# Kernel optimization log

Hardware: AMD Instinct MI355X
Metric: run time of the kernel (lower is better)

## Reference

```python
import jax, jax.numpy as jnp
import numpy as np

N_NODES = 100000
N_EDGES = 1600000
N_GRAPHS = 512
NODE_DIM = 64   # len(node_indices)
GRAPH_DIM = 16  # len(graph_indices) == graph_channels
HIDDEN = 128
OUT = 8


def setup_inputs() -> dict:
    key = jax.random.key(0)
    ks = jax.random.split(key, 12)
    x = jax.random.normal(ks[0], (N_NODES, NODE_DIM + GRAPH_DIM), dtype=jnp.float32)
    edge_index = jax.random.randint(ks[1], (2, N_EDGES), 0, N_NODES, dtype=jnp.int64)
    batch = jnp.sort(jax.random.randint(ks[2], (N_NODES,), 0, N_GRAPHS, dtype=jnp.int64))
    def lin(k, fan_in, fan_out):
        lim = 1.0 / np.sqrt(fan_in)
        return jax.random.uniform(k, (fan_in, fan_out), jnp.float32, -lim, lim)
    return {
        "x": x, "edge_index": edge_index, "batch": batch,
        "W1": lin(ks[3], NODE_DIM, HIDDEN), "b1": jnp.zeros((HIDDEN,), jnp.float32),
        "W2": lin(ks[4], HIDDEN, HIDDEN),   "b2": jnp.zeros((HIDDEN,), jnp.float32),
        "Wm1": lin(ks[5], HIDDEN + GRAPH_DIM, HIDDEN), "bm1": jnp.zeros((HIDDEN,), jnp.float32),
        "Wm2": lin(ks[6], HIDDEN, OUT), "bm2": jnp.zeros((OUT,), jnp.float32),
    }


def _gcn_conv(h_in, src, dst, W, b):
    # PyG GCNConv: h = X W; out = D^{-1/2}(A+I)D^{-1/2} h + b, deg over A+I.
    h = h_in @ W                                        # [N, H]
    deg = jnp.zeros((N_NODES,), h.dtype).at[dst].add(1.0) + 1.0  # +1 self loop
    dinv = jax.lax.rsqrt(deg)                           # [N]
    norm = dinv[src] * dinv[dst]                        # [E]
    out = jnp.zeros_like(h).at[dst].add(norm[:, None] * h[src])
    out = out + (dinv * dinv)[:, None] * h              # self-loop term
    return out + b


def _mean_pool(v, batch):
    cnt = jax.ops.segment_sum(jnp.ones((v.shape[0],), v.dtype), batch, num_segments=N_GRAPHS)
    s = jax.ops.segment_sum(v, batch, num_segments=N_GRAPHS)
    return s / jnp.maximum(cnt, 1.0)[:, None]


def reference(x, edge_index, batch, W1, b1, W2, b2, Wm1, bm1, Wm2, bm2):
    src, dst = edge_index[0], edge_index[1]
    node_t = x[:, :NODE_DIM]                 # node_indices slice
    graph_t = _mean_pool(x[:, NODE_DIM:], batch)  # graph_indices slice, pooled [G, 16]
    h = _gcn_conv(node_t, src, dst, W1, b1)
    h = jax.nn.relu(h)                       # dropout is identity in eval mode
    h = _gcn_conv(h, src, dst, W2, b2)
    g = _mean_pool(h, batch)                 # [G, H]
    g = jnp.concatenate([g, graph_t], axis=1)
    g = jax.nn.relu(g @ Wm1 + bm1)
    return g @ Wm2 + bm2                     # [G, OUT]
```

## Files before the change

### kernel.cpp

```cpp
#include <hip/hip_runtime.h>
#include <hip/hip_bf16.h>

#define N_NODES 100000
#define N_EDGES 1600000
#define N_GRAPHS 512
#define NODE_DIM 64
#define GRAPH_DIM 16
#define HIDDEN 128
#define OUT_DIM 8

#define NBUCKETS 391
#define BIN_CAP 8192
#define EPB 4096

__device__ __forceinline__ float bflo(unsigned u) { return __uint_as_float(u << 16); }
__device__ __forceinline__ float bfhi(unsigned u) { return __uint_as_float(u & 0xffff0000u); }


__global__ __launch_bounds__(256) void k_binplace(const int* __restrict__ src,
                                                  const int* __restrict__ dst,
                                                  int* __restrict__ gcur,
                                                  unsigned* __restrict__ bin) {
    __shared__ int cnt[NBUCKETS];
    __shared__ int base[NBUCKETS];
    int t = threadIdx.x;
    for (int i = t; i < NBUCKETS; i += 256) cnt[i] = 0;
    __syncthreads();
    int e0 = blockIdx.x * EPB;
#pragma unroll
    for (int k = 0; k < EPB / 256; k++) {
        int e = e0 + k * 256 + t;
        if (e < N_EDGES) atomicAdd(&cnt[dst[e] >> 8], 1);
    }
    __syncthreads();
    for (int i = t; i < NBUCKETS; i += 256) {
        int c = cnt[i];
        base[i] = (c > 0) ? atomicAdd(&gcur[i], c) : 0;
        cnt[i] = 0;
    }
    __syncthreads();
#pragma unroll
    for (int k = 0; k < EPB / 256; k++) {
        int e = e0 + k * 256 + t;
        if (e < N_EDGES) {
            int d = dst[e];
            int b = d >> 8;
            int p = atomicAdd(&cnt[b], 1);
            bin[(size_t)b * BIN_CAP + base[b] + p] = ((unsigned)src[e] << 8) | (unsigned)(d & 255);
        }
    }
}


__global__ __launch_bounds__(256) void k_degBf(const int* __restrict__ gcur,
                                               const unsigned* __restrict__ bin,
                                               int* __restrict__ degcnt,
                                               float* __restrict__ dinv,
                                               int* __restrict__ bsum) {
    __shared__ int cnt[256];
    int b = blockIdx.x, t = threadIdx.x;
    cnt[t] = 0;
    __syncthreads();
    int n = gcur[b];
    const unsigned* seg = bin + (size_t)b * BIN_CAP;
    for (int i = t; i < n; i += 256) atomicAdd(&cnt[seg[i] & 255u], 1);
    __syncthreads();
    int c = cnt[t];
    int node = b * 256 + t;
    if (node < N_NODES) {
        degcnt[node] = c;
        dinv[node] = rsqrtf((float)c + 1.0f);
    }
    __syncthreads();
    for (int o = 128; o > 0; o >>= 1) {
        if (t < o) cnt[t] += cnt[t + o];
        __syncthreads();
    }
    if (t == 0) bsum[b] = cnt[0];
}


__global__ __launch_bounds__(512) void k_scanb(const int* __restrict__ bsum,
                                               int* __restrict__ bofs) {
    __shared__ int s[512];
    int t = threadIdx.x;
    int v = (t < NBUCKETS) ? bsum[t] : 0;
    s[t] = v;
    __syncthreads();
    for (int o = 1; o < 512; o <<= 1) {
        int u = (t >= o) ? s[t - o] : 0;
        __syncthreads();
        s[t] += u;
        __syncthreads();
    }
    if (t < NBUCKETS) bofs[t] = s[t] - v;
}


__global__ __launch_bounds__(256) void k_rowfill(const int* __restrict__ degcnt,
                                                 const int* __restrict__ bofs,
                                                 const int* __restrict__ gcur,
                                                 const unsigned* __restrict__ bin,
                                                 const float* __restrict__ dinv,
                                                 int* __restrict__ row_start,
                                                 int2* __restrict__ csre,
                                                 float* __restrict__ gt_sum) {
    __shared__ int sc[256];
    __shared__ int rsl[256];
    __shared__ int cnt[256];
    __shared__ float dl[256];
    int b = blockIdx.x, t = threadIdx.x;
    if (b < 32) gt_sum[b * 256 + t] = 0.0f;
    int node = b * 256 + t;
    int v = (node < N_NODES) ? degcnt[node] : 0;
    sc[t] = v;
    __syncthreads();
    for (int o = 1; o < 256; o <<= 1) {
        int u = (t >= o) ? sc[t - o] : 0;
        __syncthreads();
        sc[t] += u;
        __syncthreads();
    }
    int rs = bofs[b] + sc[t] - v;
    if (node < N_NODES) row_start[node] = rs;
    rsl[t] = rs;
    cnt[t] = 0;
    dl[t] = rsqrtf((float)v + 1.0f);
    __syncthreads();
    int n = gcur[b];
    const unsigned* seg = bin + (size_t)b * BIN_CAP;
    for (int i = t; i < n; i += 256) {
        unsigned e = seg[i];
        int dlidx = (int)(e & 255u);
        int s = (int)(e >> 8);
        int pos = rsl[dlidx] + atomicAdd(&cnt[dlidx], 1);
        csre[pos] = make_int2(s, __float_as_int(dinv[s] * dl[dlidx]));
    }
}


__global__ __launch_bounds__(256) void k_packstat(const float* __restrict__ x,
                                                  const int* __restrict__ batch,
                                                  ushort* __restrict__ xb,
                                                  float* __restrict__ gt_sum) {
    int t = threadIdx.x;
    int i0 = blockIdx.x * 64;
    for (int idx = t; idx < 64 * 32; idx += 256) {
        int node = i0 + (idx >> 5);
        if (node < N_NODES) {
            int c2 = idx & 31;
            float2 v = *(const float2*)&x[(size_t)node * 80 + c2 * 2];
            __hip_bfloat16 lo = __float2bfloat16(v.x);
            __hip_bfloat16 hi = __float2bfloat16(v.y);
            ushort2 pv = make_ushort2(*(ushort*)&lo, *(ushort*)&hi);
            ((ushort2*)xb)[(size_t)node * 32 + c2] = pv;
        }
    }
    int c = t & 15, sub = t >> 4;
    int iend = min(i0 + 64, N_NODES);
    float acc = 0.0f;
    int g = -1;
    for (int i = i0 + sub; i < iend; i += 16) {
        int bi = batch[i];
        if (bi != g) {
            if (g >= 0) atomicAdd(&gt_sum[g * GRAPH_DIM + c], acc);
            acc = 0.0f; g = bi;
        }
        acc += x[(size_t)i * 80 + NODE_DIM + c];
    }
    if (g >= 0) atomicAdd(&gt_sum[g * GRAPH_DIM + c], acc);
}


#define LDX(s_) __uint_as_float((unsigned)xb[(size_t)(s_)*64 + lane] << 16)

__global__ __launch_bounds__(256) void k_conv1(const int2* __restrict__ csre,
                                               const int* __restrict__ row_start,
                                               const float* __restrict__ dinv,
                                               const ushort* __restrict__ xb,
                                               const float* __restrict__ W,
                                               const float* __restrict__ bias,
                                               ushort* __restrict__ C,
                                               float* __restrict__ gsum2) {
    __shared__ float zs[8][64];
    int t = threadIdx.x;
    if (blockIdx.x < 256) gsum2[blockIdx.x * 256 + t] = 0.0f;
    int w = t >> 6, lane = t & 63;
    int nA = blockIdx.x * 8 + w * 2;
    int nB = nA + 1;
    int rsA = row_start[nA], reA = (nA == N_NODES - 1) ? N_EDGES : row_start[nA + 1];
    int rsB = row_start[nB], reB = (nB == N_NODES - 1) ? N_EDGES : row_start[nB + 1];
    float aA0 = 0.f, aA1 = 0.f, aA2 = 0.f, aA3 = 0.f;
    float aB0 = 0.f, aB1 = 0.f, aB2 = 0.f, aB3 = 0.f;
    int kA = rsA, kB = rsB;
    while (kA + 4 <= reA && kB + 4 <= reB) {
        int2 eA0 = csre[kA], eA1 = csre[kA + 1], eA2 = csre[kA + 2], eA3 = csre[kA + 3];
        int2 eB0 = csre[kB], eB1 = csre[kB + 1], eB2 = csre[kB + 2], eB3 = csre[kB + 3];
        float vA0 = LDX(eA0.x), vA1 = LDX(eA1.x), vA2 = LDX(eA2.x), vA3 = LDX(eA3.x);
        float vB0 = LDX(eB0.x), vB1 = LDX(eB1.x), vB2 = LDX(eB2.x), vB3 = LDX(eB3.x);
        aA0 += __int_as_float(eA0.y) * vA0; aA1 += __int_as_float(eA1.y) * vA1;
        aA2 += __int_as_float(eA2.y) * vA2; aA3 += __int_as_float(eA3.y) * vA3;
        aB0 += __int_as_float(eB0.y) * vB0; aB1 += __int_as_float(eB1.y) * vB1;
        aB2 += __int_as_float(eB2.y) * vB2; aB3 += __int_as_float(eB3.y) * vB3;
        kA += 4; kB += 4;
    }
    while (kA + 4 <= reA) {
        int2 e0 = csre[kA], e1 = csre[kA + 1], e2 = csre[kA + 2], e3 = csre[kA + 3];
        float v0 = LDX(e0.x), v1 = LDX(e1.x), v2 = LDX(e2.x), v3 = LDX(e3.x);
        aA0 += __int_as_float(e0.y) * v0; aA1 += __int_as_float(e1.y) * v1;
        aA2 += __int_as_float(e2.y) * v2; aA3 += __int_as_float(e3.y) * v3;
        kA += 4;
    }
    while (kB + 4 <= reB) {
        int2 e0 = csre[kB], e1 = csre[kB + 1], e2 = csre[kB + 2], e3 = csre[kB + 3];
        float v0 = LDX(e0.x), v1 = LDX(e1.x), v2 = LDX(e2.x), v3 = LDX(e3.x);
        aB0 += __int_as_float(e0.y) * v0; aB1 += __int_as_float(e1.y) * v1;
        aB2 += __int_as_float(e2.y) * v2; aB3 += __int_as_float(e3.y) * v3;
        kB += 4;
    }
    while (kA < reA && kB < reB) {
        int2 eA = csre[kA]; int2 eB = csre[kB];
        aA0 += __int_as_float(eA.y) * LDX(eA.x);
        aB0 += __int_as_float(eB.y) * LDX(eB.x);
        kA++; kB++;
    }
    while (kA < reA) { int2 e = csre[kA]; aA0 += __int_as_float(e.y) * LDX(e.x); kA++; }
    while (kB < reB) { int2 e = csre[kB]; aB0 += __int_as_float(e.y) * LDX(e.x); kB++; }
    float dA = dinv[nA], dB = dinv[nB];
    zs[w * 2][lane]     = aA0 + aA1 + aA2 + aA3 + dA * dA * LDX(nA);
    zs[w * 2 + 1][lane] = aB0 + aB1 + aB2 + aB3 + dB * dB * LDX(nB);
    __syncthreads();
    if (t < 128) {
        int j = t;
        float acc[8];
#pragma unroll
        for (int m = 0; m < 8; m++) acc[m] = 0.0f;
        for (int k = 0; k < 64; k++) {
            float wv = W[k * 128 + j];
#pragma unroll
            for (int m = 0; m < 8; m++) acc[m] += zs[m][k] * wv;
        }
        float b = bias[j];
        size_t row0 = (size_t)blockIdx.x * 8;
#pragma unroll
        for (int m = 0; m < 8; m++) {
            float v = fmaxf(acc[m] + b, 0.0f);
            __hip_bfloat16 hv = __float2bfloat16(v);
            C[(row0 + m) * 128 + j] = *(ushort*)&hv;
        }
    }
}


__global__ __launch_bounds__(256) void k_gather2(const int2* __restrict__ csre,
                                                 const int* __restrict__ row_start,
                                                 const float* __restrict__ dinv,
                                                 const unsigned* __restrict__ h,
                                                 const int* __restrict__ batch,
                                                 float* __restrict__ gsum2) {
    __shared__ float2 red[8][64];
    int w = threadIdx.x >> 6, lane = threadIdx.x & 63;
    int nA = blockIdx.x * 8 + w * 2;
    int nB = nA + 1;
    int rsA = row_start[nA], reA = (nA == N_NODES - 1) ? N_EDGES : row_start[nA + 1];
    int rsB = row_start[nB], reB = (nB == N_NODES - 1) ? N_EDGES : row_start[nB + 1];
    float2 aA0 = {0.f,0.f}, aA1 = {0.f,0.f}, aA2 = {0.f,0.f}, aA3 = {0.f,0.f};
    float2 aB0 = {0.f,0.f}, aB1 = {0.f,0.f}, aB2 = {0.f,0.f}, aB3 = {0.f,0.f};
    int kA = rsA, kB = rsB;
#define FMA2(acc_, wbits_, u_) { float w_ = __int_as_float(wbits_); \
                             acc_.x += w_ * bflo(u_); acc_.y += w_ * bfhi(u_); }
    while (kA + 4 <= reA && kB + 4 <= reB) {
        int2 eA0 = csre[kA], eA1 = csre[kA + 1], eA2 = csre[kA + 2], eA3 = csre[kA + 3];
        int2 eB0 = csre[kB], eB1 = csre[kB + 1], eB2 = csre[kB + 2], eB3 = csre[kB + 3];
        unsigned uA0 = h[(size_t)eA0.x * 64 + lane], uA1 = h[(size_t)eA1.x * 64 + lane];
        unsigned uA2 = h[(size_t)eA2.x * 64 + lane], uA3 = h[(size_t)eA3.x * 64 + lane];
        unsigned uB0 = h[(size_t)eB0.x * 64 + lane], uB1 = h[(size_t)eB1.x * 64 + lane];
        unsigned uB2 = h[(size_t)eB2.x * 64 + lane], uB3 = h[(size_t)eB3.x * 64 + lane];
        FMA2(aA0, eA0.y, uA0); FMA2(aA1, eA1.y, uA1); FMA2(aA2, eA2.y, uA2); FMA2(aA3, eA3.y, uA3);
        FMA2(aB0, eB0.y, uB0); FMA2(aB1, eB1.y, uB1); FMA2(aB2, eB2.y, uB2); FMA2(aB3, eB3.y, uB3);
        kA += 4; kB += 4;
    }
    while (kA + 4 <= reA) {
        int2 e0 = csre[kA], e1 = csre[kA + 1], e2 = csre[kA + 2], e3 = csre[kA + 3];
        unsigned u0 = h[(size_t)e0.x * 64 + lane], u1 = h[(size_t)e1.x * 64 + lane];
        unsigned u2 = h[(size_t)e2.x * 64 + lane], u3 = h[(size_t)e3.x * 64 + lane];
        FMA2(aA0, e0.y, u0); FMA2(aA1, e1.y, u1); FMA2(aA2, e2.y, u2); FMA2(aA3, e3.y, u3);
        kA += 4;
    }
    while (kB + 4 <= reB) {
        int2 e0 = csre[kB], e1 = csre[kB + 1], e2 = csre[kB + 2], e3 = csre[kB + 3];
        unsigned u0 = h[(size_t)e0.x * 64 + lane], u1 = h[(size_t)e1.x * 64 + lane];
        unsigned u2 = h[(size_t)e2.x * 64 + lane], u3 = h[(size_t)e3.x * 64 + lane];
        FMA2(aB0, e0.y, u0); FMA2(aB1, e1.y, u1); FMA2(aB2, e2.y, u2); FMA2(aB3, e3.y, u3);
        kB += 4;
    }
    while (kA < reA && kB < reB) {
        int2 eA = csre[kA]; int2 eB = csre[kB];
        unsigned uA = h[(size_t)eA.x * 64 + lane], uB = h[(size_t)eB.x * 64 + lane];
        FMA2(aA0, eA.y, uA); FMA2(aB0, eB.y, uB);
        kA++; kB++;
    }
    while (kA < reA) {
        int2 e = csre[kA]; unsigned u = h[(size_t)e.x * 64 + lane];
        FMA2(aA0, e.y, u); kA++;
    }
    while (kB < reB) {
        int2 e = csre[kB]; unsigned u = h[(size_t)e.x * 64 + lane];
        FMA2(aB0, e.y, u); kB++;
    }
#undef FMA2
    float dA = dinv[nA], dB = dinv[nB];
    unsigned usA = h[(size_t)nA * 64 + lane];
    unsigned usB = h[(size_t)nB * 64 + lane];
    float2 rA, rB;
    rA.x = aA0.x + aA1.x + aA2.x + aA3.x + dA * dA * bflo(usA);
    rA.y = aA0.y + aA1.y + aA2.y + aA3.y + dA * dA * bfhi(usA);
    rB.x = aB0.x + aB1.x + aB2.x + aB3.x + dB * dB * bflo(usB);
    rB.y = aB0.y + aB1.y + aB2.y + aB3.y + dB * dB * bfhi(usB);
    red[w * 2][lane] = rA;
    red[w * 2 + 1][lane] = rB;
    __syncthreads();
    int g0 = batch[blockIdx.x * 8];
    int g7 = batch[blockIdx.x * 8 + 7];
    if (g0 == g7) {
        if (w == 0) {
            float sx = 0.f, sy = 0.f;
#pragma unroll
            for (int q = 0; q < 8; q++) { sx += red[q][lane].x; sy += red[q][lane].y; }
            atomicAdd(&gsum2[g0 * 128 + 2 * lane], sx);
            atomicAdd(&gsum2[g0 * 128 + 2 * lane + 1], sy);
        }
    } else {
        int gA = batch[nA], gB = batch[nB];
        atomicAdd(&gsum2[gA * 128 + 2 * lane], rA.x);
        atomicAdd(&gsum2[gA * 128 + 2 * lane + 1], rA.y);
        atomicAdd(&gsum2[gB * 128 + 2 * lane], rB.x);
        atomicAdd(&gsum2[gB * 128 + 2 * lane + 1], rB.y);
    }
}


__global__ __launch_bounds__(128) void k_mlp(const float* __restrict__ gsum2,
                                             const float* __restrict__ gt_sum,
                                             const int* __restrict__ batch,
                                             const float* __restrict__ W2,
                                             const float* __restrict__ b2,
                                             const float* __restrict__ Wm1,
                                             const float* __restrict__ bm1,
                                             const float* __restrict__ Wm2,
                                             const float* __restrict__ bm2,
                                             float* __restrict__ out) {
    __shared__ float srow[HIDDEN];
    __shared__ float g144[HIDDEN + GRAPH_DIM];
    __shared__ float sm[HIDDEN];
    __shared__ int cnt_sh;
    int b = blockIdx.x;
    int j = threadIdx.x;
    float raw = gsum2[b * 128 + j];
    float gtraw = (j < GRAPH_DIM) ? gt_sum[b * GRAPH_DIM + j] : 0.0f;
    if (j == 0) {
        int lo = 0, hi = N_NODES;
        while (lo < hi) { int m = (lo + hi) >> 1; if (batch[m] < b) lo = m + 1; else hi = m; }
        int a = lo;
        lo = 0; hi = N_NODES;
        while (lo < hi) { int m = (lo + hi) >> 1; if (batch[m] < b + 1) lo = m + 1; else hi = m; }
        cnt_sh = lo - a;
    }
    __syncthreads();
    float inv = 1.0f / fmaxf((float)cnt_sh, 1.0f);
    srow[j] = raw * inv;
    if (j < GRAPH_DIM) g144[128 + j] = gtraw * inv;
    __syncthreads();
    float z = b2[j];
    for (int k = 0; k < 128; k++) z += srow[k] * W2[k * 128 + j];
    g144[j] = z;
    __syncthreads();
    float acc = bm1[j];
    for (int k = 0; k < HIDDEN + GRAPH_DIM; k++) acc += g144[k] * Wm1[k * 128 + j];
    sm[j] = fmaxf(acc, 0.0f);
    __syncthreads();
    if (j < OUT_DIM) {
        float o = bm2[j];
        for (int k = 0; k < 128; k++) o += sm[k] * Wm2[k * OUT_DIM + j];
        out[b * OUT_DIM + j] = o;
    }
}

extern "C" void kernel_launch(void* const* d_in, const int* in_sizes, int n_in,
                              void* d_out, int out_size, void* d_ws, size_t ws_size,
                              hipStream_t stream) {
    const float* x    = (const float*)d_in[0];
    const int*   edge = (const int*)d_in[1];
    const int*   src  = edge;
    const int*   dst  = edge + N_EDGES;
    const int*   batch= (const int*)d_in[2];
    const float* W1   = (const float*)d_in[3];
    const float* b1   = (const float*)d_in[4];
    const float* W2   = (const float*)d_in[5];
    const float* b2   = (const float*)d_in[6];
    const float* Wm1  = (const float*)d_in[7];
    const float* bm1  = (const float*)d_in[8];
    const float* Wm2  = (const float*)d_in[9];
    const float* bm2  = (const float*)d_in[10];
    float* out = (float*)d_out;

    char* ws = (char*)d_ws;
    char* p = ws;
    unsigned* bin   = (unsigned*)p;  p += (size_t)NBUCKETS * BIN_CAP * 4;
    int2*  csre     = (int2*)p;      p += (size_t)N_EDGES * 8;
    ushort* h1b     = (ushort*)p;    p += (size_t)N_NODES * 128 * 2;
    ushort* xb      = (ushort*)p;    p += (size_t)N_NODES * 64 * 2;
    int*   degcnt   = (int*)p;       p += (size_t)NBUCKETS * 256 * 4;
    int*   row_start= (int*)p;       p += (size_t)N_NODES * 4;
    float* dinv     = (float*)p;     p += (size_t)N_NODES * 4;
    int*   gcur     = (int*)p;       p += (size_t)NBUCKETS * 4;
    int*   bsum     = (int*)p;       p += 512 * 4;
    int*   bofs     = (int*)p;       p += 512 * 4;
    float* gt_sum   = (float*)p;     p += (size_t)N_GRAPHS * GRAPH_DIM * 4;
    float* gsum2    = (float*)p;     p += (size_t)N_GRAPHS * 128 * 4;

    hipMemsetAsync(gcur, 0, (size_t)NBUCKETS * 4, stream);

    k_binplace<<<(N_EDGES + EPB - 1) / EPB, 256, 0, stream>>>(src, dst, gcur, bin);
    k_degBf<<<NBUCKETS, 256, 0, stream>>>(gcur, bin, degcnt, dinv, bsum);
    k_scanb<<<1, 512, 0, stream>>>(bsum, bofs);
    k_rowfill<<<NBUCKETS, 256, 0, stream>>>(degcnt, bofs, gcur, bin, dinv, row_start, csre, gt_sum);

    k_packstat<<<(N_NODES + 63) / 64, 256, 0, stream>>>(x, batch, xb, gt_sum);

    k_conv1<<<N_NODES / 8, 256, 0, stream>>>(csre, row_start, dinv, xb, W1, b1, h1b, gsum2);

    k_gather2<<<N_NODES / 8, 256, 0, stream>>>(csre, row_start, dinv,
                                               (const unsigned*)h1b, batch, gsum2);

    k_mlp<<<N_GRAPHS, 128, 0, stream>>>(gsum2, gt_sum, batch, W2, b2, Wm1, bm1, Wm2, bm2, out);
}
```

Before: 248.2 us.

## Fuse CSR build into one kernel with padded bucket rows and on-the-fly norms

Merges the degree count, block scan and row fill kernels into a single per-bucket build kernel. Rows now start at a fixed bucket offset (b*BIN_CAP) and are stored as start/end pairs, so no global scan is needed. The CSR stores only source indices, and the edge weight is recomputed in the gather kernels from dinv, which halves index traffic at the cost of an extra random dinv load per edge. The conv1 dense transform is also split across all 256 threads instead of 128.

Result: faster. 237.7 us (-4.2%).

```diff
diff --git a/kernel.cpp b/kernel.cpp
--- a/kernel.cpp
+++ b/kernel.cpp
@@ -52,68 +52,25 @@
 }
 
 
-__global__ __launch_bounds__(256) void k_degBf(const int* __restrict__ gcur,
+__global__ __launch_bounds__(256) void k_build(const int* __restrict__ gcur,
                                                const unsigned* __restrict__ bin,
-                                               int* __restrict__ degcnt,
                                                float* __restrict__ dinv,
-                                               int* __restrict__ bsum) {
+                                               int2* __restrict__ rowse,
+                                               int* __restrict__ csr,
+                                               float* __restrict__ gt_sum) {
     __shared__ int cnt[256];
+    __shared__ int sc[256];
+    __shared__ int rsl[256];
     int b = blockIdx.x, t = threadIdx.x;
+    if (b < 32) gt_sum[b * 256 + t] = 0.0f;
     cnt[t] = 0;
     __syncthreads();
     int n = gcur[b];
     const unsigned* seg = bin + (size_t)b * BIN_CAP;
     for (int i = t; i < n; i += 256) atomicAdd(&cnt[seg[i] & 255u], 1);
     __syncthreads();
-    int c = cnt[t];
-    int node = b * 256 + t;
-    if (node < N_NODES) {
-        degcnt[node] = c;
-        dinv[node] = rsqrtf((float)c + 1.0f);
-    }
-    __syncthreads();
-    for (int o = 128; o > 0; o >>= 1) {
-        if (t < o) cnt[t] += cnt[t + o];
-        __syncthreads();
-    }
-    if (t == 0) bsum[b] = cnt[0];
-}
-
-
-__global__ __launch_bounds__(512) void k_scanb(const int* __restrict__ bsum,
-                                               int* __restrict__ bofs) {
-    __shared__ int s[512];
-    int t = threadIdx.x;
-    int v = (t < NBUCKETS) ? bsum[t] : 0;
-    s[t] = v;
-    __syncthreads();
-    for (int o = 1; o < 512; o <<= 1) {
-        int u = (t >= o) ? s[t - o] : 0;
-        __syncthreads();
-        s[t] += u;
-        __syncthreads();
-    }
-    if (t < NBUCKETS) bofs[t] = s[t] - v;
-}
-
-
-__global__ __launch_bounds__(256) void k_rowfill(const int* __restrict__ degcnt,
-                                                 const int* __restrict__ bofs,
-                                                 const int* __restrict__ gcur,
-                                                 const unsigned* __restrict__ bin,
-                                                 const float* __restrict__ dinv,
-                                                 int* __restrict__ row_start,
-                                                 int2* __restrict__ csre,
-                                                 float* __restrict__ gt_sum) {
-    __shared__ int sc[256];
-    __shared__ int rsl[256];
-    __shared__ int cnt[256];
-    __shared__ float dl[256];
-    int b = blockIdx.x, t = threadIdx.x;
-    if (b < 32) gt_sum[b * 256 + t] = 0.0f;
-    int node = b * 256 + t;
-    int v = (node < N_NODES) ? degcnt[node] : 0;
-    sc[t] = v;
+    int deg = cnt[t];
+    sc[t] = deg;
     __syncthreads();
     for (int o = 1; o < 256; o <<= 1) {
         int u = (t >= o) ? sc[t - o] : 0;
@@ -121,20 +78,19 @@
         sc[t] += u;
         __syncthreads();
     }
-    int rs = bofs[b] + sc[t] - v;
-    if (node < N_NODES) row_start[node] = rs;
+    int rs = b * BIN_CAP + sc[t] - deg;
+    int node = b * 256 + t;
+    if (node < N_NODES) {
+        dinv[node] = rsqrtf((float)deg + 1.0f);
+        rowse[node] = make_int2(rs, rs + deg);
+    }
     rsl[t] = rs;
     cnt[t] = 0;
-    dl[t] = rsqrtf((float)v + 1.0f);
-    __syncthreads();
-    int n = gcur[b];
-    const unsigned* seg = bin + (size_t)b * BIN_CAP;
+    __syncthreads();
     for (int i = t; i < n; i += 256) {
         unsigned e = seg[i];
         int dlidx = (int)(e & 255u);
-        int s = (int)(e >> 8);
-        int pos = rsl[dlidx] + atomicAdd(&cnt[dlidx], 1);
-        csre[pos] = make_int2(s, __float_as_int(dinv[s] * dl[dlidx]));
+        csr[rsl[dlidx] + atomicAdd(&cnt[dlidx], 1)] = (int)(e >> 8);
     }
 }
 
@@ -174,8 +130,8 @@
 
 #define LDX(s_) __uint_as_float((unsigned)xb[(size_t)(s_)*64 + lane] << 16)
 
-__global__ __launch_bounds__(256) void k_conv1(const int2* __restrict__ csre,
-                                               const int* __restrict__ row_start,
+__global__ __launch_bounds__(256) void k_conv1(const int* __restrict__ csr,
+                                               const int2* __restrict__ rowse,
                                                const float* __restrict__ dinv,
                                                const ushort* __restrict__ xb,
                                                const float* __restrict__ W,
@@ -188,62 +144,64 @@
     int w = t >> 6, lane = t & 63;
     int nA = blockIdx.x * 8 + w * 2;
     int nB = nA + 1;
-    int rsA = row_start[nA], reA = (nA == N_NODES - 1) ? N_EDGES : row_start[nA + 1];
-    int rsB = row_start[nB], reB = (nB == N_NODES - 1) ? N_EDGES : row_start[nB + 1];
+    int2 seA = rowse[nA];
+    int2 seB = rowse[nB];
+    int kA = seA.x, reA = seA.y;
+    int kB = seB.x, reB = seB.y;
+    float dA = dinv[nA], dB = dinv[nB];
     float aA0 = 0.f, aA1 = 0.f, aA2 = 0.f, aA3 = 0.f;
     float aB0 = 0.f, aB1 = 0.f, aB2 = 0.f, aB3 = 0.f;
-    int kA = rsA, kB = rsB;
     while (kA + 4 <= reA && kB + 4 <= reB) {
-        int2 eA0 = csre[kA], eA1 = csre[kA + 1], eA2 = csre[kA + 2], eA3 = csre[kA + 3];
-        int2 eB0 = csre[kB], eB1 = csre[kB + 1], eB2 = csre[kB + 2], eB3 = csre[kB + 3];
-        float vA0 = LDX(eA0.x), vA1 = LDX(eA1.x), vA2 = LDX(eA2.x), vA3 = LDX(eA3.x);
-        float vB0 = LDX(eB0.x), vB1 = LDX(eB1.x), vB2 = LDX(eB2.x), vB3 = LDX(eB3.x);
-        aA0 += __int_as_float(eA0.y) * vA0; aA1 += __int_as_float(eA1.y) * vA1;
-        aA2 += __int_as_float(eA2.y) * vA2; aA3 += __int_as_float(eA3.y) * vA3;
-        aB0 += __int_as_float(eB0.y) * vB0; aB1 += __int_as_float(eB1.y) * vB1;
-        aB2 += __int_as_float(eB2.y) * vB2; aB3 += __int_as_float(eB3.y) * vB3;
+        int a0 = csr[kA], a1 = csr[kA + 1], a2 = csr[kA + 2], a3 = csr[kA + 3];
+        int b0 = csr[kB], b1 = csr[kB + 1], b2 = csr[kB + 2], b3 = csr[kB + 3];
+        float wa0 = dinv[a0] * dA, wa1 = dinv[a1] * dA, wa2 = dinv[a2] * dA, wa3 = dinv[a3] * dA;
+        float wb0 = dinv[b0] * dB, wb1 = dinv[b1] * dB, wb2 = dinv[b2] * dB, wb3 = dinv[b3] * dB;
+        float vA0 = LDX(a0), vA1 = LDX(a1), vA2 = LDX(a2), vA3 = LDX(a3);
+        float vB0 = LDX(b0), vB1 = LDX(b1), vB2 = LDX(b2), vB3 = LDX(b3);
+        aA0 += wa0 * vA0; aA1 += wa1 * vA1; aA2 += wa2 * vA2; aA3 += wa3 * vA3;
+        aB0 += wb0 * vB0; aB1 += wb1 * vB1; aB2 += wb2 * vB2; aB3 += wb3 * vB3;
         kA += 4; kB += 4;
     }
     while (kA + 4 <= reA) {
-        int2 e0 = csre[kA], e1 = csre[kA + 1], e2 = csre[kA + 2], e3 = csre[kA + 3];
-        float v0 = LDX(e0.x), v1 = LDX(e1.x), v2 = LDX(e2.x), v3 = LDX(e3.x);
-        aA0 += __int_as_float(e0.y) * v0; aA1 += __int_as_float(e1.y) * v1;
-        aA2 += __int_as_float(e2.y) * v2; aA3 += __int_as_float(e3.y) * v3;
+        int a0 = csr[kA], a1 = csr[kA + 1], a2 = csr[kA + 2], a3 = csr[kA + 3];
+        float wa0 = dinv[a0] * dA, wa1 = dinv[a1] * dA, wa2 = dinv[a2] * dA, wa3 = dinv[a3] * dA;
+        float v0 = LDX(a0), v1 = LDX(a1), v2 = LDX(a2), v3 = LDX(a3);
+        aA0 += wa0 * v0; aA1 += wa1 * v1; aA2 += wa2 * v2; aA3 += wa3 * v3;
         kA += 4;
     }
     while (kB + 4 <= reB) {
-        int2 e0 = csre[kB], e1 = csre[kB + 1], e2 = csre[kB + 2], e3 = csre[kB + 3];
-        float v0 = LDX(e0.x), v1 = LDX(e1.x), v2 = LDX(e2.x), v3 = LDX(e3.x);
-        aB0 += __int_as_float(e0.y) * v0; aB1 += __int_as_float(e1.y) * v1;
-        aB2 += __int_as_float(e2.y) * v2; aB3 += __int_as_float(e3.y) * v3;
+        int b0 = csr[kB], b1 = csr[kB + 1], b2 = csr[kB + 2], b3 = csr[kB + 3];
+        float wb0 = dinv[b0] * dB, wb1 = dinv[b1] * dB, wb2 = dinv[b2] * dB, wb3 = dinv[b3] * dB;
+        float v0 = LDX(b0), v1 = LDX(b1), v2 = LDX(b2), v3 = LDX(b3);
+        aB0 += wb0 * v0; aB1 += wb1 * v1; aB2 += wb2 * v2; aB3 += wb3 * v3;
         kB += 4;
     }
     while (kA < reA && kB < reB) {
-        int2 eA = csre[kA]; int2 eB = csre[kB];
-        aA0 += __int_as_float(eA.y) * LDX(eA.x);
-        aB0 += __int_as_float(eB.y) * LDX(eB.x);
+        int a0 = csr[kA]; int b0 = csr[kB];
+        aA0 += dinv[a0] * dA * LDX(a0);
+        aB0 += dinv[b0] * dB * LDX(b0);
         kA++; kB++;
     }
-    while (kA < reA) { int2 e = csre[kA]; aA0 += __int_as_float(e.y) * LDX(e.x); kA++; }
-    while (kB < reB) { int2 e = csre[kB]; aB0 += __int_as_float(e.y) * LDX(e.x); kB++; }
-    float dA = dinv[nA], dB = dinv[nB];
+    while (kA < reA) { int a0 = csr[kA]; aA0 += dinv[a0] * dA * LDX(a0); kA++; }
+    while (kB < reB) { int b0 = csr[kB]; aB0 += dinv[b0] * dB * LDX(b0); kB++; }
     zs[w * 2][lane]     = aA0 + aA1 + aA2 + aA3 + dA * dA * LDX(nA);
     zs[w * 2 + 1][lane] = aB0 + aB1 + aB2 + aB3 + dB * dB * LDX(nB);
     __syncthreads();
-    if (t < 128) {
-        int j = t;
-        float acc[8];
-#pragma unroll
-        for (int m = 0; m < 8; m++) acc[m] = 0.0f;
+    {
+        int j = t & 127;
+        int hf = t >> 7;
+        float acc[4];
+#pragma unroll
+        for (int m = 0; m < 4; m++) acc[m] = 0.0f;
         for (int k = 0; k < 64; k++) {
-            float wv = W[k * 128 + j];
-#pragma unroll
-            for (int m = 0; m < 8; m++) acc[m] += zs[m][k] * wv;
+            float wk = W[k * 128 + j];
+#pragma unroll
+            for (int m = 0; m < 4; m++) acc[m] += zs[hf * 4 + m][k] * wk;
         }
         float b = bias[j];
-        size_t row0 = (size_t)blockIdx.x * 8;
-#pragma unroll
-        for (int m = 0; m < 8; m++) {
+        size_t row0 = (size_t)blockIdx.x * 8 + hf * 4;
+#pragma unroll
+        for (int m = 0; m < 4; m++) {
             float v = fmaxf(acc[m] + b, 0.0f);
             __hip_bfloat16 hv = __float2bfloat16(v);
             C[(row0 + m) * 128 + j] = *(ushort*)&hv;
@@ -252,8 +210,8 @@
 }
 
 
-__global__ __launch_bounds__(256) void k_gather2(const int2* __restrict__ csre,
-                                                 const int* __restrict__ row_start,
+__global__ __launch_bounds__(256) void k_gather2(const int* __restrict__ csr,
+                                                 const int2* __restrict__ rowse,
                                                  const float* __restrict__ dinv,
                                                  const unsigned* __restrict__ h,
                                                  const int* __restrict__ batch,
@@ -262,54 +220,61 @@
     int w = threadIdx.x >> 6, lane = threadIdx.x & 63;
     int nA = blockIdx.x * 8 + w * 2;
     int nB = nA + 1;
-    int rsA = row_start[nA], reA = (nA == N_NODES - 1) ? N_EDGES : row_start[nA + 1];
-    int rsB = row_start[nB], reB = (nB == N_NODES - 1) ? N_EDGES : row_start[nB + 1];
+    int2 seA = rowse[nA];
+    int2 seB = rowse[nB];
+    int kA = seA.x, reA = seA.y;
+    int kB = seB.x, reB = seB.y;
+    float dA = dinv[nA], dB = dinv[nB];
     float2 aA0 = {0.f,0.f}, aA1 = {0.f,0.f}, aA2 = {0.f,0.f}, aA3 = {0.f,0.f};
     float2 aB0 = {0.f,0.f}, aB1 = {0.f,0.f}, aB2 = {0.f,0.f}, aB3 = {0.f,0.f};
-    int kA = rsA, kB = rsB;
-#define FMA2(acc_, wbits_, u_) { float w_ = __int_as_float(wbits_); \
-                             acc_.x += w_ * bflo(u_); acc_.y += w_ * bfhi(u_); }
+#define FMA2(acc_, w_, u_) { acc_.x += (w_) * bflo(u_); acc_.y += (w_) * bfhi(u_); }
     while (kA + 4 <= reA && kB + 4 <= reB) {
-        int2 eA0 = csre[kA], eA1 = csre[kA + 1], eA2 = csre[kA + 2], eA3 = csre[kA + 3];
-        int2 eB0 = csre[kB], eB1 = csre[kB + 1], eB2 = csre[kB + 2], eB3 = csre[kB + 3];
-        unsigned uA0 = h[(size_t)eA0.x * 64 + lane], uA1 = h[(size_t)eA1.x * 64 + lane];
-        unsigned uA2 = h[(size_t)eA2.x * 64 + lane], uA3 = h[(size_t)eA3.x * 64 + lane];
-        unsigned uB0 = h[(size_t)eB0.x * 64 + lane], uB1 = h[(size_t)eB1.x * 64 + lane];
-        unsigned uB2 = h[(size_t)eB2.x * 64 + lane], uB3 = h[(size_t)eB3.x * 64 + lane];
-        FMA2(aA0, eA0.y, uA0); FMA2(aA1, eA1.y, uA1); FMA2(aA2, eA2.y, uA2); FMA2(aA3, eA3.y, uA3);
-        FMA2(aB0, eB0.y, uB0); FMA2(aB1, eB1.y, uB1); FMA2(aB2, eB2.y, uB2); FMA2(aB3, eB3.y, uB3);
+        int a0 = csr[kA], a1 = csr[kA + 1], a2 = csr[kA + 2], a3 = csr[kA + 3];
+        int b0 = csr[kB], b1 = csr[kB + 1], b2 = csr[kB + 2], b3 = csr[kB + 3];
+        float wa0 = dinv[a0] * dA, wa1 = dinv[a1] * dA, wa2 = dinv[a2] * dA, wa3 = dinv[a3] * dA;
+        float wb0 = dinv[b0] * dB, wb1 = dinv[b1] * dB, wb2 = dinv[b2] * dB, wb3 = dinv[b3] * dB;
+        unsigned uA0 = h[(size_t)a0 * 64 + lane], uA1 = h[(size_t)a1 * 64 + lane];
+        unsigned uA2 = h[(size_t)a2 * 64 + lane], uA3 = h[(size_t)a3 * 64 + lane];
+        unsigned uB0 = h[(size_t)b0 * 64 + lane], uB1 = h[(size_t)b1 * 64 + lane];
+        unsigned uB2 = h[(size_t)b2 * 64 + lane], uB3 = h[(size_t)b3 * 64 + lane];
+        FMA2(aA0, wa0, uA0); FMA2(aA1, wa1, uA1); FMA2(aA2, wa2, uA2); FMA2(aA3, wa3, uA3);
+        FMA2(aB0, wb0, uB0); FMA2(aB1, wb1, uB1); FMA2(aB2, wb2, uB2); FMA2(aB3, wb3, uB3);
         kA += 4; kB += 4;
     }
     while (kA + 4 <= reA) {
-        int2 e0 = csre[kA], e1 = csre[kA + 1], e2 = csre[kA + 2], e3 = csre[kA + 3];
-        unsigned u0 = h[(size_t)e0.x * 64 + lane], u1 = h[(size_t)e1.x * 64 + lane];
-        unsigned u2 = h[(size_t)e2.x * 64 + lane], u3 = h[(size_t)e3.x * 64 + lane];
-        FMA2(aA0, e0.y, u0); FMA2(aA1, e1.y, u1); FMA2(aA2, e2.y, u2); FMA2(aA3, e3.y, u3);
+        int a0 = csr[kA], a1 = csr[kA + 1], a2 = csr[kA + 2], a3 = csr[kA + 3];
+        float wa0 = dinv[a0] * dA, wa1 = dinv[a1] * dA, wa2 = dinv[a2] * dA, wa3 = dinv[a3] * dA;
+        unsigned u0 = h[(size_t)a0 * 64 + lane], u1 = h[(size_t)a1 * 64 + lane];
+        unsigned u2 = h[(size_t)a2 * 64 + lane], u3 = h[(size_t)a3 * 64 + lane];
+        FMA2(aA0, wa0, u0); FMA2(aA1, wa1, u1); FMA2(aA2, wa2, u2); FMA2(aA3, wa3, u3);
         kA += 4;
     }
     while (kB + 4 <= reB) {
-        int2 e0 = csre[kB], e1 = csre[kB + 1], e2 = csre[kB + 2], e3 = csre[kB + 3];
-        unsigned u0 = h[(size_t)e0.x * 64 + lane], u1 = h[(size_t)e1.x * 64 + lane];
-        unsigned u2 = h[(size_t)e2.x * 64 + lane], u3 = h[(size_t)e3.x * 64 + lane];
-        FMA2(aB0, e0.y, u0); FMA2(aB1, e1.y, u1); FMA2(aB2, e2.y, u2); FMA2(aB3, e3.y, u3);
+        int b0 = csr[kB], b1 = csr[kB + 1], b2 = csr[kB + 2], b3 = csr[kB + 3];
+        float wb0 = dinv[b0] * dB, wb1 = dinv[b1] * dB, wb2 = dinv[b2] * dB, wb3 = dinv[b3] * dB;
+        unsigned u0 = h[(size_t)b0 * 64 + lane], u1 = h[(size_t)b1 * 64 + lane];
+        unsigned u2 = h[(size_t)b2 * 64 + lane], u3 = h[(size_t)b3 * 64 + lane];
+        FMA2(aB0, wb0, u0); FMA2(aB1, wb1, u1); FMA2(aB2, wb2, u2); FMA2(aB3, wb3, u3);
         kB += 4;
     }
     while (kA < reA && kB < reB) {
-        int2 eA = csre[kA]; int2 eB = csre[kB];
-        unsigned uA = h[(size_t)eA.x * 64 + lane], uB = h[(size_t)eB.x * 64 + lane];
-        FMA2(aA0, eA.y, uA); FMA2(aB0, eB.y, uB);
+        int a0 = csr[kA]; int b0 = csr[kB];
+        float wa0 = dinv[a0] * dA, wb0 = dinv[b0] * dB;
+        unsigned uA = h[(size_t)a0 * 64 + lane], uB = h[(size_t)b0 * 64 + lane];
+        FMA2(aA0, wa0, uA); FMA2(aB0, wb0, uB);
         kA++; kB++;
     }
     while (kA < reA) {
-        int2 e = csre[kA]; unsigned u = h[(size_t)e.x * 64 + lane];
-        FMA2(aA0, e.y, u); kA++;
+        int a0 = csr[kA];
+        unsigned u = h[(size_t)a0 * 64 + lane];
+        FMA2(aA0, dinv[a0] * dA, u); kA++;
     }
     while (kB < reB) {
-        int2 e = csre[kB]; unsigned u = h[(size_t)e.x * 64 + lane];
-        FMA2(aB0, e.y, u); kB++;
+        int b0 = csr[kB];
+        unsigned u = h[(size_t)b0 * 64 + lane];
+        FMA2(aB0, dinv[b0] * dB, u); kB++;
     }
 #undef FMA2
-    float dA = dinv[nA], dB = dinv[nB];
     unsigned usA = h[(size_t)nA * 64 + lane];
     unsigned usB = h[(size_t)nB * 64 + lane];
     float2 rA, rB;
@@ -407,30 +372,25 @@
     char* ws = (char*)d_ws;
     char* p = ws;
     unsigned* bin   = (unsigned*)p;  p += (size_t)NBUCKETS * BIN_CAP * 4;
-    int2*  csre     = (int2*)p;      p += (size_t)N_EDGES * 8;
+    int*   csr      = (int*)p;       p += (size_t)NBUCKETS * BIN_CAP * 4;
     ushort* h1b     = (ushort*)p;    p += (size_t)N_NODES * 128 * 2;
     ushort* xb      = (ushort*)p;    p += (size_t)N_NODES * 64 * 2;
-    int*   degcnt   = (int*)p;       p += (size_t)NBUCKETS * 256 * 4;
-    int*   row_start= (int*)p;       p += (size_t)N_NODES * 4;
+    int2*  rowse    = (int2*)p;      p += (size_t)N_NODES * 8;
     float* dinv     = (float*)p;     p += (size_t)N_NODES * 4;
     int*   gcur     = (int*)p;       p += (size_t)NBUCKETS * 4;
-    int*   bsum     = (int*)p;       p += 512 * 4;
-    int*   bofs     = (int*)p;       p += 512 * 4;
     float* gt_sum   = (float*)p;     p += (size_t)N_GRAPHS * GRAPH_DIM * 4;
     float* gsum2    = (float*)p;     p += (size_t)N_GRAPHS * 128 * 4;
 
     hipMemsetAsync(gcur, 0, (size_t)NBUCKETS * 4, stream);
 
     k_binplace<<<(N_EDGES + EPB - 1) / EPB, 256, 0, stream>>>(src, dst, gcur, bin);
-    k_degBf<<<NBUCKETS, 256, 0, stream>>>(gcur, bin, degcnt, dinv, bsum);
-    k_scanb<<<1, 512, 0, stream>>>(bsum, bofs);
-    k_rowfill<<<NBUCKETS, 256, 0, stream>>>(degcnt, bofs, gcur, bin, dinv, row_start, csre, gt_sum);
+    k_build<<<NBUCKETS, 256, 0, stream>>>(gcur, bin, dinv, rowse, csr, gt_sum);
 
     k_packstat<<<(N_NODES + 63) / 64, 256, 0, stream>>>(x, batch, xb, gt_sum);
 
-    k_conv1<<<N_NODES / 8, 256, 0, stream>>>(csre, row_start, dinv, xb, W1, b1, h1b, gsum2);
-
-    k_gather2<<<N_NODES / 8, 256, 0, stream>>>(csre, row_start, dinv,
+    k_conv1<<<N_NODES / 8, 256, 0, stream>>>(csr, rowse, dinv, xb, W1, b1, h1b, gsum2);
+
+    k_gather2<<<N_NODES / 8, 256, 0, stream>>>(csr, rowse, dinv,
                                                (const unsigned*)h1b, batch, gsum2);
 
     k_mlp<<<N_GRAPHS, 128, 0, stream>>>(gsum2, gt_sum, batch, W2, b2, Wm1, bm1, Wm2, bm2, out);
```
